# Optimization experiments

Measured on AMD Instinct MI355X. Metric: run time of the kernel, lower is better.

The kernel has to match this reference:

```python
import jax, jax.numpy as jnp
import numpy as np

B, S, D, H = 4, 4096, 1024, 128

def setup_inputs() -> dict:
    key = jax.random.key(0)
    ks = jax.random.split(key, 4)
    scale = 1.0 / np.sqrt(D)
    return {
        "x":  jax.random.normal(ks[0], (B, S, D), dtype=jnp.float32),
        "Wq": jax.random.normal(ks[1], (D, H), dtype=jnp.float32) * scale,
        "bq": jnp.zeros((H,), dtype=jnp.float32),
        "Wk": jax.random.normal(ks[2], (D, H), dtype=jnp.float32) * scale,
        "bk": jnp.zeros((H,), dtype=jnp.float32),
        "Wv": jax.random.normal(ks[3], (D, H), dtype=jnp.float32) * scale,
        "bv": jnp.zeros((H,), dtype=jnp.float32),
    }

def reference(x, Wq, bq, Wk, bk, Wv, bv):
    # q, k, v: [B, S, H]
    q = x @ Wq + bq
    k = x @ Wk + bk
    v = x @ Wv + bv
    inv_sqrt_h = 1.0 / jnp.sqrt(jnp.asarray(q.shape[-1], q.dtype))
    # scores: [B, S, S]
    scores = jnp.einsum('bqh,bkh->bqk', q, k) * inv_sqrt_h
    seq = q.shape[1]
    causal = jnp.tril(jnp.ones((seq, seq), dtype=bool))
    scores = jnp.where(causal, scores, jnp.asarray(-jnp.inf, scores.dtype))
    probs = jax.nn.softmax(scores, axis=-1)
    # dropout p=0.0 -> identity
    return jnp.einsum('bqk,bkh->bqh', probs, v)
```

## Files before the change

kernel.cpp:

```cpp
#include <hip/hip_runtime.h>
#include <hip/hip_bf16.h>

#define B_ 4
#define S_ 4096
#define D_ 1024
#define H_ 128

typedef _Float16 half8 __attribute__((ext_vector_type(8)));
typedef _Float16 half4v __attribute__((ext_vector_type(4)));
typedef float float4v __attribute__((ext_vector_type(4)));


__device__ __forceinline__ void gload_lds16(const void* g, void* l) {
    __builtin_amdgcn_global_load_lds(
        (const __attribute__((address_space(1))) unsigned int*)g,
        (__attribute__((address_space(3))) unsigned int*)l, 16, 0, 0);
}

__global__ __launch_bounds__(256) void k_cvt_w(const float* __restrict__ Wq,
                                               const float* __restrict__ Wk,
                                               const float* __restrict__ Wv,
                                               _Float16* __restrict__ WT) {
    const float* W = blockIdx.y == 0 ? Wq : (blockIdx.y == 1 ? Wk : Wv);
    int idx = blockIdx.x * 256 + threadIdx.x;
    int k = idx >> 7, n = idx & 127;
    WT[(size_t)blockIdx.y * (H_ * D_) + (size_t)n * D_ + k] = (_Float16)W[idx];
}

__global__ __launch_bounds__(256, 3) void k_proj(const float* __restrict__ X,
                                                 const _Float16* __restrict__ WT,
                                                 const float* __restrict__ bq,
                                                 const float* __restrict__ bk,
                                                 const float* __restrict__ bv,
                                                 _Float16* __restrict__ Qf,
                                                 _Float16* __restrict__ Kz,
                                                 _Float16* __restrict__ Vz) {
    __shared__ char smem[32768];
    char* AsB = smem;
    char* BsB = smem + 16384;

    const int t    = threadIdx.x;
    const int bid  = blockIdx.x;
    const int w    = bid >> 8;
    const int m0   = (bid & 255) * 64;
    const int lane = t & 63, wid = t >> 6;
    const int lo   = lane & 15, hi = lane >> 4;
    const int wr   = wid >> 1, wc = wid & 1;

    const _Float16* Wt = WT + (size_t)w * (H_ * D_);

    const int raj = wid * 16 + (lane >> 4);
    const int rbj = wid * 32 + (lane >> 3);
    const int ca0 = (lane & 15) * 4;
    const int cb0 = (lane & 7) * 8;

    float4v acc[2][4];
#pragma unroll
    for (int mt = 0; mt < 2; ++mt)
#pragma unroll
        for (int nt = 0; nt < 4; ++nt) acc[mt][nt] = {0.f, 0.f, 0.f, 0.f};

    for (int it = 0; it < 16; ++it) {
        const int k0 = it * 64;
#pragma unroll
        for (int j = 0; j < 4; ++j) {
            const int ra = raj + j * 4;
            const int ca = ca0 ^ ((ra & 7) * 4);
            gload_lds16(X + (size_t)(m0 + ra) * D_ + k0 + ca,
                        AsB + (wid * 16 + j * 4) * 256);
            const int rb = rbj + j * 8;
            const int cb = cb0 ^ ((rb & 7) * 8);
            gload_lds16(Wt + (size_t)rb * D_ + k0 + cb,
                        BsB + (wid * 32 + j * 8) * 128);
        }
        __syncthreads();
#pragma unroll
        for (int kk = 0; kk < 2; ++kk) {
            const int cb = kk * 32 + hi * 8;
            half8 af[2];
#pragma unroll
            for (int mt = 0; mt < 2; ++mt) {
                const int r = wr * 32 + mt * 16 + lo;
                const int v = (r & 7) * 4;
                float4v a0 = *(const float4v*)(AsB + r * 256 + ((cb ^ v) << 2));
                float4v a1 = *(const float4v*)(AsB + r * 256 + (((cb + 4) ^ v) << 2));
                half8 h;
                h[0]=(_Float16)a0[0]; h[1]=(_Float16)a0[1]; h[2]=(_Float16)a0[2]; h[3]=(_Float16)a0[3];
                h[4]=(_Float16)a1[0]; h[5]=(_Float16)a1[1]; h[6]=(_Float16)a1[2]; h[7]=(_Float16)a1[3];
                af[mt] = h;
            }
            half8 bf[4];
#pragma unroll
            for (int nt = 0; nt < 4; ++nt) {
                const int rb2 = wc * 64 + nt * 16 + lo;
                const int vb  = (rb2 & 7) * 8;
                bf[nt] = *(const half8*)(BsB + rb2 * 128 + (((cb) ^ vb) << 1));
            }
#pragma unroll
            for (int mt = 0; mt < 2; ++mt)
#pragma unroll
                for (int nt = 0; nt < 4; ++nt)
                    acc[mt][nt] = __builtin_amdgcn_mfma_f32_16x16x32_f16(
                        af[mt], bf[nt], acc[mt][nt], 0, 0, 0);
        }
        __syncthreads();
    }

    const float* bias = (w == 0) ? bq : ((w == 1) ? bk : bv);
    const float scale = (w == 0) ? (0.08838834764831845f * 1.4426950408889634f) : 1.0f;
    _Float16* Ct = (_Float16*)smem;
#pragma unroll
    for (int mt = 0; mt < 2; ++mt)
#pragma unroll
        for (int nt = 0; nt < 4; ++nt) {
            const int col   = wc * 64 + nt * 16 + lo;
            const float bn  = bias[col];
            const int rbase = wr * 32 + mt * 16 + 4 * hi;
#pragma unroll
            for (int j = 0; j < 4; ++j)
                Ct[(rbase + j) * 136 + col] = (_Float16)((acc[mt][nt][j] + bn) * scale);
        }
    __syncthreads();

    const int bb  = m0 >> 12;
    const int tt0 = (m0 & (S_ - 1)) >> 5;

    if (w == 0) {
        const int r = t >> 2, c0 = (t & 3) * 32;
        _Float16* dst = Qf + (size_t)(m0 + r) * H_ + c0;
        const _Float16* srcp = &Ct[r * 136 + c0];
#pragma unroll
        for (int cc = 0; cc < 4; ++cc)
            *(half8*)(dst + cc * 8) = *(const half8*)(srcp + cc * 8);
    } else if (w == 1) {
        const int rowp = ((lo >> 2) << 3) + (lo & 3);
#pragma unroll
        for (int q = 0; q < 4; ++q) {
            const int fid = wid * 4 + q;
            const int ft = fid >> 3, k2 = (fid >> 1) & 3, c = fid & 1;
            const int row = ft * 32 + rowp + 4 * c;
            half8 v = *(const half8*)(&Ct[row * 136 + k2 * 32 + hi * 8]);
            *(half8*)(Kz + (size_t)(bb * 128 + tt0 + ft) * 4096 +
                      (k2 * 2 + c) * 512 + lane * 8) = v;
        }
    } else {
#pragma unroll
        for (int q = 0; q < 4; ++q) {
            const int fid = wid * 4 + q;
            const int ft = fid >> 3, hc = fid & 7;
            half8 v;
#pragma unroll
            for (int e = 0; e < 8; ++e)
                v[e] = Ct[(ft * 32 + hi * 8 + e) * 136 + hc * 16 + lo];
            *(half8*)(Vz + (size_t)(bb * 128 + tt0 + ft) * 4096 +
                      hc * 512 + lane * 8) = v;
        }
    }
}

__global__ __launch_bounds__(512, 2) void k_attn(const _Float16* __restrict__ Qf,
                                                 const _Float16* __restrict__ Kz,
                                                 const _Float16* __restrict__ Vz,
                                                 float* __restrict__ Out) {
    __shared__ float    sm_l[8][32];
    __shared__ _Float16 sm_o[8][32][136];

    const int t    = threadIdx.x;
    const int lane = t & 63, wid = t >> 6;
    const int lo = lane & 15, hi = lane >> 4;

    const int i   = blockIdx.x;
    const int b   = (i >> 1) & 3;
    const int qtr = ((i >> 3) << 1) | (i & 1);
    const int qt  = (qtr < 64) ? qtr : (191 - qtr);
    const int q0  = qt << 5;

    const _Float16* Qb = Qf + (size_t)b * (S_ * H_);
    const _Float16* Kb = Kz + (size_t)b * 524288;
    const _Float16* Vb = Vz + (size_t)b * 524288;

    half8 qfa[4], qfb[4];
#pragma unroll
    for (int kk = 0; kk < 4; ++kk) {
        qfa[kk] = *(const half8*)(Qb + (size_t)(q0 + lo) * H_ + kk * 32 + hi * 8);
        qfb[kk] = *(const half8*)(Qb + (size_t)(q0 + 16 + lo) * H_ + kk * 32 + hi * 8);
    }

    float4v oa[8], ob[8];
#pragma unroll
    for (int hc = 0; hc < 8; ++hc) { oa[hc] = {0.f,0.f,0.f,0.f}; ob[hc] = {0.f,0.f,0.f,0.f}; }
    float la = 0.f, lb = 0.f;

    const int lane8 = lane * 8;
    const int ntiles = qt + 1;

    half8 kc0[4], kc1[4];
    if (wid < ntiles) {
        const _Float16* Kt = Kb + (size_t)wid * 4096 + lane8;
#pragma unroll
        for (int kk = 0; kk < 4; ++kk) {
            kc0[kk] = *(const half8*)(Kt + (kk * 2    ) * 512);
            kc1[kk] = *(const half8*)(Kt + (kk * 2 + 1) * 512);
        }
    }

    for (int tt = wid; tt < ntiles; tt += 8) {
        const _Float16* Vt = Vb + (size_t)tt * 4096 + lane8;
        half8 vf[8];
#pragma unroll
        for (int hc = 0; hc < 8; ++hc)
            vf[hc] = *(const half8*)(Vt + hc * 512);
        const int tn = (tt + 8 < ntiles) ? (tt + 8) : tt;
        half8 kn0[4], kn1[4];
        {
            const _Float16* Ktn = Kb + (size_t)tn * 4096 + lane8;
#pragma unroll
            for (int kk = 0; kk < 4; ++kk) {
                kn0[kk] = *(const half8*)(Ktn + (kk * 2    ) * 512);
                kn1[kk] = *(const half8*)(Ktn + (kk * 2 + 1) * 512);
            }
        }
        float4v s0a = {0.f,0.f,0.f,0.f}, s1a = {0.f,0.f,0.f,0.f};
        float4v s0b = {0.f,0.f,0.f,0.f}, s1b = {0.f,0.f,0.f,0.f};
#pragma unroll
        for (int kk = 0; kk < 4; ++kk) {
            s0a = __builtin_amdgcn_mfma_f32_16x16x32_f16(kc0[kk], qfa[kk], s0a, 0, 0, 0);
            s0b = __builtin_amdgcn_mfma_f32_16x16x32_f16(kc0[kk], qfb[kk], s0b, 0, 0, 0);
            s1a = __builtin_amdgcn_mfma_f32_16x16x32_f16(kc1[kk], qfa[kk], s1a, 0, 0, 0);
            s1b = __builtin_amdgcn_mfma_f32_16x16x32_f16(kc1[kk], qfb[kk], s1b, 0, 0, 0);
        }
        if (tt == qt) {
#pragma unroll
            for (int j = 0; j < 4; ++j) {
                const int c0 = 8 * hi + j, c1 = 8 * hi + 4 + j;
                if (c0 > lo)      s0a[j] = -INFINITY;
                if (c1 > lo)      s1a[j] = -INFINITY;
                if (c0 > 16 + lo) s0b[j] = -INFINITY;
                if (c1 > 16 + lo) s1b[j] = -INFINITY;
            }
        }
        float pa0 = __builtin_amdgcn_exp2f(s0a[0]), pa1 = __builtin_amdgcn_exp2f(s0a[1]);
        float pa2 = __builtin_amdgcn_exp2f(s0a[2]), pa3 = __builtin_amdgcn_exp2f(s0a[3]);
        float pa4 = __builtin_amdgcn_exp2f(s1a[0]), pa5 = __builtin_amdgcn_exp2f(s1a[1]);
        float pa6 = __builtin_amdgcn_exp2f(s1a[2]), pa7 = __builtin_amdgcn_exp2f(s1a[3]);
        float pb0 = __builtin_amdgcn_exp2f(s0b[0]), pb1 = __builtin_amdgcn_exp2f(s0b[1]);
        float pb2 = __builtin_amdgcn_exp2f(s0b[2]), pb3 = __builtin_amdgcn_exp2f(s0b[3]);
        float pb4 = __builtin_amdgcn_exp2f(s1b[0]), pb5 = __builtin_amdgcn_exp2f(s1b[1]);
        float pb6 = __builtin_amdgcn_exp2f(s1b[2]), pb7 = __builtin_amdgcn_exp2f(s1b[3]);
        la += ((pa0+pa1)+(pa2+pa3)) + ((pa4+pa5)+(pa6+pa7));
        lb += ((pb0+pb1)+(pb2+pb3)) + ((pb4+pb5)+(pb6+pb7));
        half8 pfa, pfb;
        pfa[0]=(_Float16)pa0; pfa[1]=(_Float16)pa1; pfa[2]=(_Float16)pa2; pfa[3]=(_Float16)pa3;
        pfa[4]=(_Float16)pa4; pfa[5]=(_Float16)pa5; pfa[6]=(_Float16)pa6; pfa[7]=(_Float16)pa7;
        pfb[0]=(_Float16)pb0; pfb[1]=(_Float16)pb1; pfb[2]=(_Float16)pb2; pfb[3]=(_Float16)pb3;
        pfb[4]=(_Float16)pb4; pfb[5]=(_Float16)pb5; pfb[6]=(_Float16)pb6; pfb[7]=(_Float16)pb7;
#pragma unroll
        for (int hc = 0; hc < 8; ++hc) {
            oa[hc] = __builtin_amdgcn_mfma_f32_16x16x32_f16(vf[hc], pfa, oa[hc], 0, 0, 0);
            ob[hc] = __builtin_amdgcn_mfma_f32_16x16x32_f16(vf[hc], pfb, ob[hc], 0, 0, 0);
        }
#pragma unroll
        for (int kk = 0; kk < 4; ++kk) { kc0[kk] = kn0[kk]; kc1[kk] = kn1[kk]; }
    }

    la += __shfl_xor(la, 16); la += __shfl_xor(la, 32);
    lb += __shfl_xor(lb, 16); lb += __shfl_xor(lb, 32);

    sm_l[wid][lo]      = la;
    sm_l[wid][16 + lo] = lb;
#pragma unroll
    for (int hc = 0; hc < 8; ++hc) {
        half4v va, vb;
#pragma unroll
        for (int j = 0; j < 4; ++j) { va[j] = (_Float16)oa[hc][j]; vb[j] = (_Float16)ob[hc][j]; }
        *(half4v*)(&sm_o[wid][lo][hc * 16 + 4 * hi])      = va;
        *(half4v*)(&sm_o[wid][16 + lo][hc * 16 + 4 * hi]) = vb;
    }
    __syncthreads();

#pragma unroll
    for (int qh = 0; qh < 2; ++qh) {
        const int q = qh * 16 + lo;
        float L = 0.f;
#pragma unroll
        for (int w = 0; w < 8; ++w) L += sm_l[w][q];
        const float invL = 1.f / L;
        float4v ov = {0.f, 0.f, 0.f, 0.f};
#pragma unroll
        for (int w = 0; w < 8; ++w) {
            half4v tv = *(const half4v*)(&sm_o[w][q][wid * 16 + 4 * hi]);
#pragma unroll
            for (int j = 0; j < 4; ++j) ov[j] += (float)tv[j];
        }
#pragma unroll
        for (int j = 0; j < 4; ++j) ov[j] *= invL;
        *(float4v*)(Out + ((size_t)b * S_ + q0 + q) * H_ + wid * 16 + 4 * hi) = ov;
    }
}

extern "C" void kernel_launch(void* const* d_in, const int* in_sizes, int n_in,
                              void* d_out, int out_size, void* d_ws, size_t ws_size,
                              hipStream_t stream) {
    const float* x  = (const float*)d_in[0];
    const float* Wq = (const float*)d_in[1];
    const float* bq = (const float*)d_in[2];
    const float* Wk = (const float*)d_in[3];
    const float* bk = (const float*)d_in[4];
    const float* Wv = (const float*)d_in[5];
    const float* bv = (const float*)d_in[6];
    float* out = (float*)d_out;

    char* ws = (char*)d_ws;
    _Float16* WT = (_Float16*)ws;
    _Float16* Qf = (_Float16*)(ws + 786432);
    _Float16* Kz = (_Float16*)(ws + 786432 + 4194304);
    _Float16* Vz = (_Float16*)(ws + 786432 + 8388608);

    hipLaunchKernelGGL(k_cvt_w, dim3(512, 3), dim3(256), 0, stream, Wq, Wk, Wv, WT);
    hipLaunchKernelGGL(k_proj, dim3(768), dim3(256), 0, stream,
                       x, WT, bq, bk, bv, Qf, Kz, Vz);
    hipLaunchKernelGGL(k_attn, dim3(512), dim3(512), 0, stream, Qf, Kz, Vz, out);
}
```

Before: 60.44 us.

## Double-buffer LDS tiles in QKV projection to overlap loads with MFMA

Doubles the shared-memory footprint of the projection kernel to 64KB and prefetches the next K-slice of X and the weights into the alternate buffer while the current slice is consumed by MFMAs. It uses an explicit vmcnt wait plus raw s_barrier in place of __syncthreads. The aim is to hide global-to-LDS load latency in the projection GEMM. In exchange, occupancy drops: launch bounds go from 3 to 2 blocks per CU and LDS per block doubles.

```diff
diff --git a/kernel.cpp b/kernel.cpp
--- a/kernel.cpp
+++ b/kernel.cpp
@@ -27,7 +27,7 @@
     WT[(size_t)blockIdx.y * (H_ * D_) + (size_t)n * D_ + k] = (_Float16)W[idx];
 }
 
-__global__ __launch_bounds__(256, 3) void k_proj(const float* __restrict__ X,
+__global__ __launch_bounds__(256, 2) void k_proj(const float* __restrict__ X,
                                                  const _Float16* __restrict__ WT,
                                                  const float* __restrict__ bq,
                                                  const float* __restrict__ bk,
@@ -35,9 +35,7 @@
                                                  _Float16* __restrict__ Qf,
                                                  _Float16* __restrict__ Kz,
                                                  _Float16* __restrict__ Vz) {
-    __shared__ char smem[32768];
-    char* AsB = smem;
-    char* BsB = smem + 16384;
+    __shared__ char smem[65536];
 
     const int t    = threadIdx.x;
     const int bid  = blockIdx.x;
@@ -54,26 +52,43 @@
     const int ca0 = (lane & 15) * 4;
     const int cb0 = (lane & 7) * 8;
 
+#define STAGE(buf, k0)                                                         \
+    {                                                                          \
+        char* AsB = smem + (buf) * 32768;                                      \
+        char* BsB = smem + (buf) * 32768 + 16384;                              \
+        _Pragma("unroll")                                                      \
+        for (int j = 0; j < 4; ++j) {                                          \
+            const int ra = raj + j * 4;                                        \
+            const int ca = ca0 ^ ((ra & 7) * 4);                               \
+            gload_lds16(X + (size_t)(m0 + ra) * D_ + (k0) + ca,                \
+                        AsB + (wid * 16 + j * 4) * 256);                       \
+            const int rb = rbj + j * 8;                                        \
+            const int cb = cb0 ^ ((rb & 7) * 8);                               \
+            gload_lds16(Wt + (size_t)rb * D_ + (k0) + cb,                      \
+                        BsB + (wid * 32 + j * 8) * 128);                       \
+        }                                                                      \
+    }
+
     float4v acc[2][4];
 #pragma unroll
     for (int mt = 0; mt < 2; ++mt)
 #pragma unroll
         for (int nt = 0; nt < 4; ++nt) acc[mt][nt] = {0.f, 0.f, 0.f, 0.f};
 
+    STAGE(0, 0);
+
     for (int it = 0; it < 16; ++it) {
-        const int k0 = it * 64;
-#pragma unroll
-        for (int j = 0; j < 4; ++j) {
-            const int ra = raj + j * 4;
-            const int ca = ca0 ^ ((ra & 7) * 4);
-            gload_lds16(X + (size_t)(m0 + ra) * D_ + k0 + ca,
-                        AsB + (wid * 16 + j * 4) * 256);
-            const int rb = rbj + j * 8;
-            const int cb = cb0 ^ ((rb & 7) * 8);
-            gload_lds16(Wt + (size_t)rb * D_ + k0 + cb,
-                        BsB + (wid * 32 + j * 8) * 128);
-        }
-        __syncthreads();
+        const int cur = it & 1;
+        if (it < 15) {
+            STAGE(cur ^ 1, (it + 1) * 64);
+            asm volatile("s_waitcnt vmcnt(8)" ::: "memory");
+        } else {
+            asm volatile("s_waitcnt vmcnt(0)" ::: "memory");
+        }
+        __builtin_amdgcn_sched_barrier(0);
+        __builtin_amdgcn_s_barrier();
+        const char* AsB = smem + cur * 32768;
+        const char* BsB = smem + cur * 32768 + 16384;
 #pragma unroll
         for (int kk = 0; kk < 2; ++kk) {
             const int cb = kk * 32 + hi * 8;
@@ -94,7 +109,7 @@
             for (int nt = 0; nt < 4; ++nt) {
                 const int rb2 = wc * 64 + nt * 16 + lo;
                 const int vb  = (rb2 & 7) * 8;
-                bf[nt] = *(const half8*)(BsB + rb2 * 128 + (((cb) ^ vb) << 1));
+                bf[nt] = *(const half8*)(BsB + rb2 * 128 + ((cb ^ vb) << 1));
             }
 #pragma unroll
             for (int mt = 0; mt < 2; ++mt)
@@ -103,8 +118,9 @@
                     acc[mt][nt] = __builtin_amdgcn_mfma_f32_16x16x32_f16(
                         af[mt], bf[nt], acc[mt][nt], 0, 0, 0);
         }
-        __syncthreads();
-    }
+        __builtin_amdgcn_s_barrier();
+    }
+#undef STAGE
 
     const float* bias = (w == 0) ? bq : ((w == 1) ? bk : bv);
     const float scale = (w == 0) ? (0.08838834764831845f * 1.4426950408889634f) : 1.0f;
```

Result: slower. 66.30 us (+9.7%).
